# Kernel optimization log

Measured on AMD Instinct MI355X. Metric: run time of the kernel, lower is better.

The kernel has to match this reference:

```python
import jax, jax.numpy as jnp
import numpy as np

N_ANCHORS = 10647
N_CLASSES = 80
N_OUT = 5 + N_CLASSES
N_GT = 2048
POS_IOU = 0.7
NEG_IOU = 0.3
N_SAMPLE = 256
POS_RATIO = 0.5


def _cxcy_to_corners(b):
    return jnp.concatenate([b[:, :2] - b[:, 2:4] / 2, b[:, :2] + b[:, 2:4] / 2], axis=-1)


def _iou(a, b):
    # a: [N,4] corner boxes, b: [M,4] corner boxes -> [N,M]
    lt = jnp.maximum(a[:, None, :2], b[None, :, :2])
    rb = jnp.minimum(a[:, None, 2:], b[None, :, 2:])
    wh = jnp.clip(rb - lt, 0.0)
    inter = wh[..., 0] * wh[..., 1]
    area_a = (a[:, 2] - a[:, 0]) * (a[:, 3] - a[:, 1])
    area_b = (b[:, 2] - b[:, 0]) * (b[:, 3] - b[:, 1])
    return inter / (area_a[:, None] + area_b[None, :] - inter)


def _bce_logits(x, t):
    # numerically stable BCEWithLogits, elementwise
    return jnp.maximum(x, 0.0) - x * t + jnp.log1p(jnp.exp(-jnp.abs(x)))


def _demote_first(labels, value, excess):
    # demote the first `excess` anchors (in index order) whose label == value to -1,
    # mirroring torch's nonzero()[randperm(excess)] which always hits the first
    # `excess` entries of the nonzero list
    m = labels == value
    cum = jnp.cumsum(m.astype(jnp.int32))
    return jnp.where(m & (cum <= excess), -1.0, labels)


def _generate_targets(priors, gt_boxes, gt_labels):
    ious = _iou(_cxcy_to_corners(priors[:, :4]), _cxcy_to_corners(gt_boxes))  # [N, M]
    gt_max_index = jnp.argmax(ious, axis=0)       # [M] best anchor per gt
    anchor_max_ious = jnp.max(ious, axis=1)       # [N]
    anchor_max_index = jnp.argmax(ious, axis=1)   # [N]
    labels = jnp.full((N_ANCHORS,), -1.0, dtype=ious.dtype)
    labels = labels.at[gt_max_index].set(1.0)
    labels = jnp.where(anchor_max_ious >= POS_IOU, 1.0, labels)
    labels = jnp.where(anchor_max_ious < NEG_IOU, 0.0, labels)
    n_pos_quota = int(POS_RATIO * N_SAMPLE)
    n_pos_actual = jnp.sum(labels == 1.0)
    labels = _demote_first(labels, 1.0, jnp.maximum(n_pos_actual - n_pos_quota, 0))
    n_neg_req = N_SAMPLE - jnp.sum(labels == 1.0)
    n_neg_actual = jnp.sum(labels == 0.0)
    labels = _demote_first(labels, 0.0, jnp.maximum(n_neg_actual - n_neg_req, 0))
    anchor_gt_box = gt_boxes[anchor_max_index]    # [N,4] matched gt box per anchor
    anchor_cls = gt_labels[anchor_max_index] + 5  # [N] one-hot class column per anchor
    targets = jnp.zeros((N_ANCHORS, N_OUT), dtype=gt_boxes.dtype)
    targets = targets.at[:, :4].set(anchor_gt_box)
    targets = targets.at[:, 4].set(labels)
    targets = targets.at[jnp.arange(N_ANCHORS), anchor_cls].set(1.0)
    return targets


def _forward(predictions, gt_boxes, gt_labels, priors):
    targets = _generate_targets(priors, gt_boxes, gt_labels)
    pred = predictions[0]                          # [N, N_OUT]
    labels = targets[:, 4]
    pos = (labels == 1.0).astype(pred.dtype)
    neg = (labels == 0.0).astype(pred.dtype)
    n_pos = jnp.maximum(jnp.sum(pos), 1.0)
    n_neg = jnp.maximum(jnp.sum(neg), 1.0)
    # masked-mean MSE over x,y,w,h on positive anchors
    diff2 = (pred[:, :4] - targets[:, :4]) ** 2
    loss_box = jnp.sum(pos[:, None] * diff2, axis=0) / n_pos
    loss_conf_obj = jnp.sum(pos * _bce_logits(pred[:, 4], targets[:, 4])) / n_pos
    loss_conf_nonobj = jnp.sum(neg * _bce_logits(pred[:, 4], targets[:, 4])) / n_neg
    loss_class = jnp.sum(pos[:, None] * _bce_logits(pred[:, 5:], targets[:, 5:])) / (n_pos * N_CLASSES)
    total_loss = jnp.sum(loss_box) + loss_conf_obj + loss_conf_nonobj + loss_class
    return pred, total_loss


def setup_inputs() -> dict:
    key = jax.random.key(0)
    k1, k2, k3, k4 = jax.random.split(key, 4)
    predictions = jax.random.normal(k1, (1, N_ANCHORS, N_OUT), dtype=jnp.float32)
    gt_boxes = jax.random.uniform(k2, (N_GT, 4), dtype=jnp.float32, minval=0.05, maxval=0.95)
    gt_labels = jax.random.randint(k3, (N_GT,), 0, N_CLASSES)
    priors = jax.random.uniform(k4, (N_ANCHORS, N_OUT), dtype=jnp.float32, minval=0.05, maxval=0.95)
    return {"predictions": predictions, "gt_boxes": gt_boxes, "gt_labels": gt_labels, "priors": priors}


def reference(predictions, gt_boxes, gt_labels, priors):
    return _forward(predictions, gt_boxes, gt_labels, priors)
```

## Files before the change

kernel.cpp:

```cpp
#include <hip/hip_runtime.h>
#include <math.h>

#define N_ANCH 10647
#define N_GT   2048
#define N_OUTC 85
#define PRED_ELEMS (N_ANCH * N_OUTC)
#define PRED_V4    (PRED_ELEMS / 4)
#define N_CHUNK    42

struct WS {
    unsigned long long akey[N_ANCH];
    unsigned long long gkey[N_GT];
    float4 ac[N_ANCH];
    float  aa[N_ANCH];
    float4 gc[N_GT];
    float  ga[N_GT];
    int lab[N_ANCH];
    int cnt_p[N_CHUNK], cnt_n[N_CHUNK];
    int poslist[128], poscls[128];
    float4 posbox[128];
    int neglist[256];
    int counts[2];
};

__device__ __forceinline__ float bce(float x, float t) {
    return fmaxf(x, 0.0f) - x * t + log1pf(expf(-fabsf(x)));
}

__global__ __launch_bounds__(256) void k_prep(const float* __restrict__ pred,
                                              const float* __restrict__ gtb,
                                              const float* __restrict__ priors,
                                              float* __restrict__ out,
                                              WS* __restrict__ ws) {
    int idx = blockIdx.x * 256 + threadIdx.x;
    if (idx < PRED_V4)
        ((float4*)out)[idx] = ((const float4*)pred)[idx];
    if (idx == 0) {
        out[PRED_ELEMS - 3] = pred[PRED_ELEMS - 3];
        out[PRED_ELEMS - 2] = pred[PRED_ELEMS - 2];
        out[PRED_ELEMS - 1] = pred[PRED_ELEMS - 1];
    }
    if (idx < N_ANCH) {
        ws->akey[idx] = 0ull;
        float cx = priors[idx*N_OUTC+0], cy = priors[idx*N_OUTC+1];
        float w  = priors[idx*N_OUTC+2], h  = priors[idx*N_OUTC+3];
        float4 c = make_float4(cx - w*0.5f, cy - h*0.5f, cx + w*0.5f, cy + h*0.5f);
        ws->ac[idx] = c;
        ws->aa[idx] = (c.z - c.x) * (c.w - c.y);
    }
    if (idx < N_GT) {
        ws->gkey[idx] = 0ull;
        float cx = gtb[idx*4+0], cy = gtb[idx*4+1], w = gtb[idx*4+2], h = gtb[idx*4+3];
        float4 c = make_float4(cx - w*0.5f, cy - h*0.5f, cx + w*0.5f, cy + h*0.5f);
        ws->gc[idx] = c;
        ws->ga[idx] = (c.z - c.x) * (c.w - c.y);
    }
}

__global__ __launch_bounds__(256) void k_iou(WS* __restrict__ ws) {
    __shared__ float4 sc[128];
    __shared__ float  sa[128];
    int b = blockIdx.x, tx = threadIdx.x;
    if (b < 672) {
        int bx = b % 42, by = b / 42;
        int jbase = by * 128;
        if (tx < 128) { sc[tx] = ws->gc[jbase + tx]; sa[tx] = ws->ga[jbase + tx]; }
        __syncthreads();
        int i = bx * 256 + tx;
        bool valid = (i < N_ANCH);
        float4 a = make_float4(0.f, 0.f, 0.f, 0.f);
        float aa_ = 0.f;
        if (valid) { a = ws->ac[i]; aa_ = ws->aa[i]; }
        float bi = -1.0f; int bj = 0;
#pragma unroll 4
        for (int jj = 0; jj < 128; ++jj) {
            float4 g = sc[jj]; float ga_ = sa[jj];
            float lx = fmaxf(a.x, g.x), ly = fmaxf(a.y, g.y);
            float rx = fminf(a.z, g.z), ry = fminf(a.w, g.w);
            float w  = fmaxf(rx - lx, 0.0f), h = fmaxf(ry - ly, 0.0f);
            float inter = w * h;
            float iou = inter / ((aa_ + ga_) - inter);
            bool gt = iou > bi;
            bi = gt ? iou : bi;
            bj = gt ? jj : bj;
        }
        if (valid) {
            unsigned long long key =
                ((unsigned long long)__float_as_uint(bi) << 32) |
                (unsigned)(~(unsigned)(jbase + bj));
            atomicMax(&ws->akey[i], key);
        }
    } else {
        int b2 = b - 672;
        int bx = b2 % 8, by = b2 / 8;
        int ibase = by * 128;
        if (tx < 128) {
            int i = ibase + tx;
            if (i < N_ANCH) { sc[tx] = ws->ac[i]; sa[tx] = ws->aa[i]; }
            else { sc[tx] = make_float4(0.f, 0.f, 0.f, 0.f); sa[tx] = 0.f; }
        }
        __syncthreads();
        int j = bx * 256 + tx;
        float4 g = ws->gc[j]; float ga_ = ws->ga[j];
        float bi = -1.0f; int bii = 0;
#pragma unroll 4
        for (int ii = 0; ii < 128; ++ii) {
            float4 a = sc[ii]; float aa_ = sa[ii];
            float lx = fmaxf(a.x, g.x), ly = fmaxf(a.y, g.y);
            float rx = fminf(a.z, g.z), ry = fminf(a.w, g.w);
            float w  = fmaxf(rx - lx, 0.0f), h = fmaxf(ry - ly, 0.0f);
            float inter = w * h;
            float iou = inter / ((aa_ + ga_) - inter);
            bool gt = iou > bi;
            bi = gt ? iou : bi;
            bii = gt ? ii : bii;
        }
        unsigned long long key =
            ((unsigned long long)__float_as_uint(bi) << 32) |
            (unsigned)(~(unsigned)(ibase + bii));
        atomicMax(&ws->gkey[j], key);
    }
}

__global__ __launch_bounds__(256) void k_label(WS* __restrict__ ws) {
    __shared__ int flg[256];
    __shared__ int wp[4], wn[4];
    int b = blockIdx.x, t = threadIdx.x, base = b * 256;
    int lane = t & 63, wid = t >> 6;
    flg[t] = 0;
    __syncthreads();
    for (int j = t; j < N_GT; j += 256) {
        int ai = (int)(~(unsigned)(ws->gkey[j]));
        int rel = ai - base;
        if ((unsigned)rel < 256u) flg[rel] = 1;
    }
    __syncthreads();
    int i = base + t;
    int lab = -2;
    if (i < N_ANCH) {
        float amax = __uint_as_float((unsigned)(ws->akey[i] >> 32));
        lab = (amax < 0.3f) ? 0 : ((amax >= 0.7f || flg[t]) ? 1 : -1);
        ws->lab[i] = lab;
    }
    unsigned long long b1 = __ballot(lab == 1), b0 = __ballot(lab == 0);
    if (lane == 0) { wp[wid] = __popcll(b1); wn[wid] = __popcll(b0); }
    __syncthreads();
    if (t == 0) {
        ws->cnt_p[b] = wp[0] + wp[1] + wp[2] + wp[3];
        ws->cnt_n[b] = wn[0] + wn[1] + wn[2] + wn[3];
    }
}

__global__ __launch_bounds__(256) void k_compact(const float* __restrict__ gtb,
                                                 const int* __restrict__ gtl,
                                                 WS* __restrict__ ws) {
    __shared__ int wps[4], wns[4];
    int b = blockIdx.x, t = threadIdx.x, lane = t & 63, wid = t >> 6;
    int npa = 0, nna = 0, pb = 0, nb = 0;
    for (int c = 0; c < N_CHUNK; ++c) {
        int cp = ws->cnt_p[c], cn = ws->cnt_n[c];
        if (c < b) { pb += cp; nb += cn; }
        npa += cp; nna += cn;
    }
    int excess_pos = (npa > 128) ? (npa - 128) : 0;
    int n_pos_f = npa - excess_pos;
    int n_neg_req = 256 - n_pos_f;
    int excess_neg = (nna > n_neg_req) ? (nna - n_neg_req) : 0;
    int n_neg_f = nna - excess_neg;

    int i = b * 256 + t;
    int lab = (i < N_ANCH) ? ws->lab[i] : -2;
    bool f1 = (lab == 1), f0 = (lab == 0);
    unsigned long long b1 = __ballot(f1), b0 = __ballot(f0);
    unsigned long long pm = (2ull << lane) - 1ull;
    int r1 = __popcll(b1 & pm), r0 = __popcll(b0 & pm);
    if (lane == 0) { wps[wid] = __popcll(b1); wns[wid] = __popcll(b0); }
    __syncthreads();
    int p1 = 0, p0 = 0;
    for (int w = 0; w < wid; ++w) { p1 += wps[w]; p0 += wns[w]; }
    if (f1) {
        int cum = pb + p1 + r1;
        if (cum > excess_pos) {
            int slot = cum - excess_pos - 1;
            ws->poslist[slot] = i;
            unsigned am = ~(unsigned)(ws->akey[i]);
            ws->poscls[slot] = gtl[am] + 5;
            ws->posbox[slot] = ((const float4*)gtb)[am];
        }
    }
    if (f0) {
        int cum = nb + p0 + r0;
        if (cum > excess_neg) ws->neglist[cum - excess_neg - 1] = i;
    }
    if (b == 0 && t == 0) { ws->counts[0] = n_pos_f; ws->counts[1] = n_neg_f; }
}

__global__ __launch_bounds__(1024) void k_loss(const float* __restrict__ pred,
                                               WS* __restrict__ ws,
                                               float* __restrict__ out) {
    __shared__ float fr[48];
    int tid = threadIdx.x, lane = tid & 63, wid = tid >> 6;
    int np = ws->counts[0], nn = ws->counts[1];
    float acc_a = 0.f, acc_c = 0.f, acc_n = 0.f;
    int nterms = np * N_OUTC;
    for (int t = tid; t < nterms; t += 1024) {
        int pi = t / N_OUTC, col = t - pi * N_OUTC;
        int i = ws->poslist[pi];
        float p = pred[i * N_OUTC + col];
        if (col < 4) {
            float d = p - ((const float*)&ws->posbox[pi])[col];
            acc_a += d * d;
        } else if (col == 4) {
            acc_a += bce(p, 1.0f);
        } else {
            acc_c += bce(p, (col == ws->poscls[pi]) ? 1.0f : 0.0f);
        }
    }
    for (int t = tid; t < nn; t += 1024) {
        acc_n += bce(pred[ws->neglist[t] * N_OUTC + 4], 0.0f);
    }
    for (int o = 32; o; o >>= 1) {
        acc_a += __shfl_down(acc_a, o);
        acc_c += __shfl_down(acc_c, o);
        acc_n += __shfl_down(acc_n, o);
    }
    if (lane == 0) { fr[wid] = acc_a; fr[16 + wid] = acc_c; fr[32 + wid] = acc_n; }
    __syncthreads();
    if (tid == 0) {
        float A = 0.f, C = 0.f, Nn = 0.f;
        for (int w = 0; w < 16; ++w) { A += fr[w]; C += fr[16 + w]; Nn += fr[32 + w]; }
        float npf = fmaxf((float)np, 1.0f);
        float nnf = fmaxf((float)nn, 1.0f);
        out[PRED_ELEMS] = A / npf + Nn / nnf + C / (npf * 80.0f);
    }
}

extern "C" void kernel_launch(void* const* d_in, const int* in_sizes, int n_in,
                              void* d_out, int out_size, void* d_ws, size_t ws_size,
                              hipStream_t stream) {
    const float* pred   = (const float*)d_in[0];
    const float* gtb    = (const float*)d_in[1];
    const int*   gtl    = (const int*)d_in[2];
    const float* priors = (const float*)d_in[3];
    float* out = (float*)d_out;
    WS* ws = (WS*)d_ws;

    k_prep<<<dim3((PRED_V4 + 255) / 256), 256, 0, stream>>>(pred, gtb, priors, out, ws);
    k_iou<<<dim3(672 + 672), 256, 0, stream>>>(ws);
    k_label<<<dim3(N_CHUNK), 256, 0, stream>>>(ws);
    k_compact<<<dim3(N_CHUNK), 256, 0, stream>>>(gtb, gtl, ws);
    k_loss<<<1, 1024, 0, stream>>>(pred, ws, out);
}
```

Before: 74.49 us.

## Fuse prep into IoU kernel, fuse compaction with loss, memset workspace

Folds the prediction copy and box-corner conversion into the IoU kernel, so corners are computed on the fly from priors and gt boxes instead of going through workspace arrays. Each IoU thread now handles two anchors or two gts, which halves the block count and reuses each shared-memory load. The compaction and loss kernels are merged: each selected anchor computes its loss terms directly, and the last-finishing block reduces the partials through atomics. This removes two launches and the single-block loss kernel, at the cost of a memset, float atomics with an order-dependent sum, and less parallelism per positive row.

New measurement: 88.15 us. +18.3%, slower.

```diff
diff --git a/kernel.cpp b/kernel.cpp
--- a/kernel.cpp
+++ b/kernel.cpp
@@ -7,118 +7,144 @@
 #define PRED_ELEMS (N_ANCH * N_OUTC)
 #define PRED_V4    (PRED_ELEMS / 4)
 #define N_CHUNK    42
+#define NBLK_IOU   672
+#define CPY_PER_BLK 337
 
 struct WS {
     unsigned long long akey[N_ANCH];
     unsigned long long gkey[N_GT];
-    float4 ac[N_ANCH];
-    float  aa[N_ANCH];
-    float4 gc[N_GT];
-    float  ga[N_GT];
     int lab[N_ANCH];
     int cnt_p[N_CHUNK], cnt_n[N_CHUNK];
-    int poslist[128], poscls[128];
-    float4 posbox[128];
-    int neglist[256];
-    int counts[2];
+    float acc[3];
+    unsigned int done;
 };
 
 __device__ __forceinline__ float bce(float x, float t) {
     return fmaxf(x, 0.0f) - x * t + log1pf(expf(-fabsf(x)));
 }
 
-__global__ __launch_bounds__(256) void k_prep(const float* __restrict__ pred,
-                                              const float* __restrict__ gtb,
-                                              const float* __restrict__ priors,
-                                              float* __restrict__ out,
-                                              WS* __restrict__ ws) {
-    int idx = blockIdx.x * 256 + threadIdx.x;
-    if (idx < PRED_V4)
-        ((float4*)out)[idx] = ((const float4*)pred)[idx];
-    if (idx == 0) {
+__device__ __forceinline__ unsigned long long packkey(float iou, int idx) {
+    return ((unsigned long long)__float_as_uint(iou) << 32) |
+           (unsigned)(~(unsigned)idx);
+}
+
+__global__ __launch_bounds__(256) void k_iou(const float* __restrict__ pred,
+                                             const float* __restrict__ gtb,
+                                             const float* __restrict__ priors,
+                                             float* __restrict__ out,
+                                             WS* __restrict__ ws) {
+    int b = blockIdx.x, t = threadIdx.x;
+    for (int k = t; k < CPY_PER_BLK; k += 256) {
+        int idx = b * CPY_PER_BLK + k;
+        if (idx < PRED_V4)
+            ((float4*)out)[idx] = ((const float4*)pred)[idx];
+    }
+    if (b == 0 && t == 0) {
         out[PRED_ELEMS - 3] = pred[PRED_ELEMS - 3];
         out[PRED_ELEMS - 2] = pred[PRED_ELEMS - 2];
         out[PRED_ELEMS - 1] = pred[PRED_ELEMS - 1];
     }
-    if (idx < N_ANCH) {
-        ws->akey[idx] = 0ull;
-        float cx = priors[idx*N_OUTC+0], cy = priors[idx*N_OUTC+1];
-        float w  = priors[idx*N_OUTC+2], h  = priors[idx*N_OUTC+3];
-        float4 c = make_float4(cx - w*0.5f, cy - h*0.5f, cx + w*0.5f, cy + h*0.5f);
-        ws->ac[idx] = c;
-        ws->aa[idx] = (c.z - c.x) * (c.w - c.y);
-    }
-    if (idx < N_GT) {
-        ws->gkey[idx] = 0ull;
-        float cx = gtb[idx*4+0], cy = gtb[idx*4+1], w = gtb[idx*4+2], h = gtb[idx*4+3];
-        float4 c = make_float4(cx - w*0.5f, cy - h*0.5f, cx + w*0.5f, cy + h*0.5f);
-        ws->gc[idx] = c;
-        ws->ga[idx] = (c.z - c.x) * (c.w - c.y);
-    }
-}
-
-__global__ __launch_bounds__(256) void k_iou(WS* __restrict__ ws) {
+
     __shared__ float4 sc[128];
     __shared__ float  sa[128];
-    int b = blockIdx.x, tx = threadIdx.x;
-    if (b < 672) {
-        int bx = b % 42, by = b / 42;
+
+    if (b < 336) {
+        int bx = b % 21, by = b / 21;
         int jbase = by * 128;
-        if (tx < 128) { sc[tx] = ws->gc[jbase + tx]; sa[tx] = ws->ga[jbase + tx]; }
+        if (t < 128) {
+            float4 v = ((const float4*)gtb)[jbase + t];
+            float4 c = make_float4(v.x - v.z*0.5f, v.y - v.w*0.5f,
+                                   v.x + v.z*0.5f, v.y + v.w*0.5f);
+            sc[t] = c;
+            sa[t] = (c.z - c.x) * (c.w - c.y);
+        }
+        int i0 = bx * 512 + t, i1 = i0 + 256;
+        bool v0 = (i0 < N_ANCH), v1 = (i1 < N_ANCH);
+        float4 a0 = make_float4(0.f,0.f,0.f,0.f), a1 = a0;
+        float aa0 = 0.f, aa1 = 0.f;
+        if (v0) {
+            float cx = priors[i0*N_OUTC+0], cy = priors[i0*N_OUTC+1];
+            float w  = priors[i0*N_OUTC+2], h  = priors[i0*N_OUTC+3];
+            a0 = make_float4(cx - w*0.5f, cy - h*0.5f, cx + w*0.5f, cy + h*0.5f);
+            aa0 = (a0.z - a0.x) * (a0.w - a0.y);
+        }
+        if (v1) {
+            float cx = priors[i1*N_OUTC+0], cy = priors[i1*N_OUTC+1];
+            float w  = priors[i1*N_OUTC+2], h  = priors[i1*N_OUTC+3];
+            a1 = make_float4(cx - w*0.5f, cy - h*0.5f, cx + w*0.5f, cy + h*0.5f);
+            aa1 = (a1.z - a1.x) * (a1.w - a1.y);
+        }
         __syncthreads();
-        int i = bx * 256 + tx;
-        bool valid = (i < N_ANCH);
-        float4 a = make_float4(0.f, 0.f, 0.f, 0.f);
-        float aa_ = 0.f;
-        if (valid) { a = ws->ac[i]; aa_ = ws->aa[i]; }
-        float bi = -1.0f; int bj = 0;
+        float bi0 = -1.0f, bi1 = -1.0f;
+        int bj0 = 0, bj1 = 0;
 #pragma unroll 4
         for (int jj = 0; jj < 128; ++jj) {
-            float4 g = sc[jj]; float ga_ = sa[jj];
-            float lx = fmaxf(a.x, g.x), ly = fmaxf(a.y, g.y);
-            float rx = fminf(a.z, g.z), ry = fminf(a.w, g.w);
-            float w  = fmaxf(rx - lx, 0.0f), h = fmaxf(ry - ly, 0.0f);
-            float inter = w * h;
-            float iou = inter / ((aa_ + ga_) - inter);
-            bool gt = iou > bi;
-            bi = gt ? iou : bi;
-            bj = gt ? jj : bj;
-        }
-        if (valid) {
-            unsigned long long key =
-                ((unsigned long long)__float_as_uint(bi) << 32) |
-                (unsigned)(~(unsigned)(jbase + bj));
-            atomicMax(&ws->akey[i], key);
-        }
+            float4 g = sc[jj]; float ga = sa[jj];
+            float lx0 = fmaxf(a0.x, g.x), ly0 = fmaxf(a0.y, g.y);
+            float rx0 = fminf(a0.z, g.z), ry0 = fminf(a0.w, g.w);
+            float w0 = fmaxf(rx0 - lx0, 0.f), h0 = fmaxf(ry0 - ly0, 0.f);
+            float in0 = w0 * h0;
+            float iou0 = in0 / ((aa0 + ga) - in0);
+            float lx1 = fmaxf(a1.x, g.x), ly1 = fmaxf(a1.y, g.y);
+            float rx1 = fminf(a1.z, g.z), ry1 = fminf(a1.w, g.w);
+            float w1 = fmaxf(rx1 - lx1, 0.f), h1 = fmaxf(ry1 - ly1, 0.f);
+            float in1 = w1 * h1;
+            float iou1 = in1 / ((aa1 + ga) - in1);
+            bool g0 = iou0 > bi0;
+            bi0 = g0 ? iou0 : bi0; bj0 = g0 ? jj : bj0;
+            bool g1 = iou1 > bi1;
+            bi1 = g1 ? iou1 : bi1; bj1 = g1 ? jj : bj1;
+        }
+        if (v0) atomicMax(&ws->akey[i0], packkey(bi0, jbase + bj0));
+        if (v1) atomicMax(&ws->akey[i1], packkey(bi1, jbase + bj1));
     } else {
-        int b2 = b - 672;
-        int bx = b2 % 8, by = b2 / 8;
+        int b2 = b - 336;
+        int bx = b2 % 4, by = b2 / 4;
         int ibase = by * 128;
-        if (tx < 128) {
-            int i = ibase + tx;
-            if (i < N_ANCH) { sc[tx] = ws->ac[i]; sa[tx] = ws->aa[i]; }
-            else { sc[tx] = make_float4(0.f, 0.f, 0.f, 0.f); sa[tx] = 0.f; }
-        }
+        if (t < 128) {
+            int i = ibase + t;
+            float4 c = make_float4(0.f,0.f,0.f,0.f);
+            float ar = 0.f;
+            if (i < N_ANCH) {
+                float cx = priors[i*N_OUTC+0], cy = priors[i*N_OUTC+1];
+                float w  = priors[i*N_OUTC+2], h  = priors[i*N_OUTC+3];
+                c = make_float4(cx - w*0.5f, cy - h*0.5f, cx + w*0.5f, cy + h*0.5f);
+                ar = (c.z - c.x) * (c.w - c.y);
+            }
+            sc[t] = c; sa[t] = ar;
+        }
+        int j0 = bx * 512 + t, j1 = j0 + 256;
+        float4 v = ((const float4*)gtb)[j0];
+        float4 g0 = make_float4(v.x - v.z*0.5f, v.y - v.w*0.5f,
+                                v.x + v.z*0.5f, v.y + v.w*0.5f);
+        float ga0 = (g0.z - g0.x) * (g0.w - g0.y);
+        v = ((const float4*)gtb)[j1];
+        float4 g1 = make_float4(v.x - v.z*0.5f, v.y - v.w*0.5f,
+                                v.x + v.z*0.5f, v.y + v.w*0.5f);
+        float ga1 = (g1.z - g1.x) * (g1.w - g1.y);
         __syncthreads();
-        int j = bx * 256 + tx;
-        float4 g = ws->gc[j]; float ga_ = ws->ga[j];
-        float bi = -1.0f; int bii = 0;
+        float bi0 = -1.0f, bi1 = -1.0f;
+        int bii0 = 0, bii1 = 0;
 #pragma unroll 4
         for (int ii = 0; ii < 128; ++ii) {
-            float4 a = sc[ii]; float aa_ = sa[ii];
-            float lx = fmaxf(a.x, g.x), ly = fmaxf(a.y, g.y);
-            float rx = fminf(a.z, g.z), ry = fminf(a.w, g.w);
-            float w  = fmaxf(rx - lx, 0.0f), h = fmaxf(ry - ly, 0.0f);
-            float inter = w * h;
-            float iou = inter / ((aa_ + ga_) - inter);
-            bool gt = iou > bi;
-            bi = gt ? iou : bi;
-            bii = gt ? ii : bii;
-        }
-        unsigned long long key =
-            ((unsigned long long)__float_as_uint(bi) << 32) |
-            (unsigned)(~(unsigned)(ibase + bii));
-        atomicMax(&ws->gkey[j], key);
+            float4 a = sc[ii]; float aa = sa[ii];
+            float lx0 = fmaxf(a.x, g0.x), ly0 = fmaxf(a.y, g0.y);
+            float rx0 = fminf(a.z, g0.z), ry0 = fminf(a.w, g0.w);
+            float w0 = fmaxf(rx0 - lx0, 0.f), h0 = fmaxf(ry0 - ly0, 0.f);
+            float in0 = w0 * h0;
+            float iou0 = in0 / ((aa + ga0) - in0);
+            float lx1 = fmaxf(a.x, g1.x), ly1 = fmaxf(a.y, g1.y);
+            float rx1 = fminf(a.z, g1.z), ry1 = fminf(a.w, g1.w);
+            float w1 = fmaxf(rx1 - lx1, 0.f), h1 = fmaxf(ry1 - ly1, 0.f);
+            float in1 = w1 * h1;
+            float iou1 = in1 / ((aa + ga1) - in1);
+            bool c0 = iou0 > bi0;
+            bi0 = c0 ? iou0 : bi0; bii0 = c0 ? ii : bii0;
+            bool c1 = iou1 > bi1;
+            bi1 = c1 ? iou1 : bi1; bii1 = c1 ? ii : bii1;
+        }
+        atomicMax(&ws->gkey[j0], packkey(bi0, ibase + bii0));
+        atomicMax(&ws->gkey[j1], packkey(bi1, ibase + bii1));
     }
 }
 
@@ -151,10 +177,13 @@
     }
 }
 
-__global__ __launch_bounds__(256) void k_compact(const float* __restrict__ gtb,
-                                                 const int* __restrict__ gtl,
-                                                 WS* __restrict__ ws) {
+__global__ __launch_bounds__(256) void k_closs(const float* __restrict__ pred,
+                                               const float* __restrict__ gtb,
+                                               const int* __restrict__ gtl,
+                                               WS* __restrict__ ws,
+                                               float* __restrict__ out) {
     __shared__ int wps[4], wns[4];
+    __shared__ float red[12];
     int b = blockIdx.x, t = threadIdx.x, lane = t & 63, wid = t >> 6;
     int npa = 0, nna = 0, pb = 0, nb = 0;
     for (int c = 0; c < N_CHUNK; ++c) {
@@ -171,67 +200,53 @@
     int i = b * 256 + t;
     int lab = (i < N_ANCH) ? ws->lab[i] : -2;
     bool f1 = (lab == 1), f0 = (lab == 0);
-    unsigned long long b1 = __ballot(f1), b0 = __ballot(f0);
+    unsigned long long b1 = __ballot(f1), b0v = __ballot(f0);
     unsigned long long pm = (2ull << lane) - 1ull;
-    int r1 = __popcll(b1 & pm), r0 = __popcll(b0 & pm);
-    if (lane == 0) { wps[wid] = __popcll(b1); wns[wid] = __popcll(b0); }
+    int r1 = __popcll(b1 & pm), r0 = __popcll(b0v & pm);
+    if (lane == 0) { wps[wid] = __popcll(b1); wns[wid] = __popcll(b0v); }
     __syncthreads();
     int p1 = 0, p0 = 0;
     for (int w = 0; w < wid; ++w) { p1 += wps[w]; p0 += wns[w]; }
-    if (f1) {
-        int cum = pb + p1 + r1;
-        if (cum > excess_pos) {
-            int slot = cum - excess_pos - 1;
-            ws->poslist[slot] = i;
-            unsigned am = ~(unsigned)(ws->akey[i]);
-            ws->poscls[slot] = gtl[am] + 5;
-            ws->posbox[slot] = ((const float4*)gtb)[am];
-        }
-    }
-    if (f0) {
-        int cum = nb + p0 + r0;
-        if (cum > excess_neg) ws->neglist[cum - excess_neg - 1] = i;
-    }
-    if (b == 0 && t == 0) { ws->counts[0] = n_pos_f; ws->counts[1] = n_neg_f; }
-}
-
-__global__ __launch_bounds__(1024) void k_loss(const float* __restrict__ pred,
-                                               WS* __restrict__ ws,
-                                               float* __restrict__ out) {
-    __shared__ float fr[48];
-    int tid = threadIdx.x, lane = tid & 63, wid = tid >> 6;
-    int np = ws->counts[0], nn = ws->counts[1];
+
     float acc_a = 0.f, acc_c = 0.f, acc_n = 0.f;
-    int nterms = np * N_OUTC;
-    for (int t = tid; t < nterms; t += 1024) {
-        int pi = t / N_OUTC, col = t - pi * N_OUTC;
-        int i = ws->poslist[pi];
-        float p = pred[i * N_OUTC + col];
-        if (col < 4) {
-            float d = p - ((const float*)&ws->posbox[pi])[col];
-            acc_a += d * d;
-        } else if (col == 4) {
-            acc_a += bce(p, 1.0f);
-        } else {
-            acc_c += bce(p, (col == ws->poscls[pi]) ? 1.0f : 0.0f);
-        }
-    }
-    for (int t = tid; t < nn; t += 1024) {
-        acc_n += bce(pred[ws->neglist[t] * N_OUTC + 4], 0.0f);
+    if (f1 && (pb + p1 + r1) > excess_pos) {
+        unsigned am = ~(unsigned)(ws->akey[i]);
+        float4 box = ((const float4*)gtb)[am];
+        int cls = gtl[am] + 5;
+        const float* pr = pred + i * N_OUTC;
+        float d0 = pr[0] - box.x, d1 = pr[1] - box.y;
+        float d2 = pr[2] - box.z, d3 = pr[3] - box.w;
+        acc_a = d0*d0 + d1*d1 + d2*d2 + d3*d3 + bce(pr[4], 1.0f);
+        for (int c = 5; c < N_OUTC; ++c)
+            acc_c += bce(pr[c], (c == cls) ? 1.0f : 0.0f);
+    }
+    if (f0 && (nb + p0 + r0) > excess_neg) {
+        acc_n = bce(pred[i * N_OUTC + 4], 0.0f);
     }
     for (int o = 32; o; o >>= 1) {
         acc_a += __shfl_down(acc_a, o);
         acc_c += __shfl_down(acc_c, o);
         acc_n += __shfl_down(acc_n, o);
     }
-    if (lane == 0) { fr[wid] = acc_a; fr[16 + wid] = acc_c; fr[32 + wid] = acc_n; }
-    __syncthreads();
-    if (tid == 0) {
-        float A = 0.f, C = 0.f, Nn = 0.f;
-        for (int w = 0; w < 16; ++w) { A += fr[w]; C += fr[16 + w]; Nn += fr[32 + w]; }
-        float npf = fmaxf((float)np, 1.0f);
-        float nnf = fmaxf((float)nn, 1.0f);
-        out[PRED_ELEMS] = A / npf + Nn / nnf + C / (npf * 80.0f);
+    if (lane == 0) { red[wid] = acc_a; red[4 + wid] = acc_c; red[8 + wid] = acc_n; }
+    __syncthreads();
+    if (t == 0) {
+        float A = red[0] + red[1] + red[2] + red[3];
+        float C = red[4] + red[5] + red[6] + red[7];
+        float Nn = red[8] + red[9] + red[10] + red[11];
+        atomicAdd(&ws->acc[0], A);
+        atomicAdd(&ws->acc[1], C);
+        atomicAdd(&ws->acc[2], Nn);
+        __threadfence();
+        unsigned old = atomicAdd(&ws->done, 1u);
+        if (old == N_CHUNK - 1) {
+            float Af = atomicAdd(&ws->acc[0], 0.0f);
+            float Cf = atomicAdd(&ws->acc[1], 0.0f);
+            float Nf = atomicAdd(&ws->acc[2], 0.0f);
+            float np = fmaxf((float)n_pos_f, 1.0f);
+            float nn = fmaxf((float)n_neg_f, 1.0f);
+            out[PRED_ELEMS] = Af / np + Nf / nn + Cf / (np * 80.0f);
+        }
     }
 }
 
@@ -245,9 +260,8 @@
     float* out = (float*)d_out;
     WS* ws = (WS*)d_ws;
 
-    k_prep<<<dim3((PRED_V4 + 255) / 256), 256, 0, stream>>>(pred, gtb, priors, out, ws);
-    k_iou<<<dim3(672 + 672), 256, 0, stream>>>(ws);
+    hipMemsetAsync(d_ws, 0, sizeof(WS), stream);
+    k_iou<<<dim3(NBLK_IOU), 256, 0, stream>>>(pred, gtb, priors, out, ws);
     k_label<<<dim3(N_CHUNK), 256, 0, stream>>>(ws);
-    k_compact<<<dim3(N_CHUNK), 256, 0, stream>>>(gtb, gtl, ws);
-    k_loss<<<1, 1024, 0, stream>>>(pred, ws, out);
-}
+    k_closs<<<dim3(N_CHUNK), 256, 0, stream>>>(pred, gtb, gtl, ws, out);
+}
```
